# Optimization experiments

Measured on AMD Instinct MI355X. Metric: run time of the kernel, lower is better.

Reference implementation:

```python
import jax, jax.numpy as jnp
import numpy as np

BATCH, IN, OUT = 8192, 4096, 4096


def setup_inputs() -> dict:
    key = jax.random.key(0)
    k1, k2, k3 = jax.random.split(key, 3)
    x = jax.random.normal(k1, (BATCH, IN), dtype=jnp.float32)
    weight = jax.random.normal(k2, (OUT, IN), dtype=jnp.float32)
    bias = jax.random.normal(k3, (OUT,), dtype=jnp.float32)
    return {"x": x, "weight": weight, "bias": bias}


def reference(x, weight, bias):
    # Binarize weights/bias with sign (matches torch.sign: sign(0)=0), then fp32 GEMM + bias add.
    w = jnp.sign(weight)            # [OUT, IN], values in {-1, 0, +1}
    b = jnp.sign(bias)              # [OUT]
    return jnp.dot(x, w.T) + b[None, :]   # [BATCH, OUT]
```

## Files before the change

### kernel.cpp

```cpp
#include <hip/hip_runtime.h>
#include <stdint.h>
#include <stddef.h>


#define MDIM 8192
#define NDIM 4096
#define KDIM 4096
#define NT   (KDIM / 64)

typedef __attribute__((ext_vector_type(8))) short bf16x8;
typedef __attribute__((ext_vector_type(4))) float f32x4;

__device__ __forceinline__ short f2bf(float f) {
  union { float f; unsigned u; } a; a.f = f;
  unsigned r = a.u + 0x7FFFu + ((a.u >> 16) & 1u);
  return (short)(r >> 16);
}

__device__ __forceinline__ float fsign(float x) {
  return (x > 0.f) ? 1.f : ((x < 0.f) ? -1.f : 0.f);
}

__device__ __forceinline__ short signbf(float x) {
  return (x > 0.f) ? (short)0x3F80 : ((x < 0.f) ? (short)0xBF80 : (short)0);
}

__device__ __forceinline__ void gl_lds16(const void* g, void* l) {
  __builtin_amdgcn_global_load_lds(
      (const __attribute__((address_space(1))) unsigned*)g,
      (__attribute__((address_space(3))) unsigned*)l,
      16, 0, 0);
}


__global__ void cvt_x_kernel(const float* __restrict__ x, short* __restrict__ o) {
  int i = blockIdx.x * blockDim.x + threadIdx.x;
  float4 v = ((const float4*)x)[i];
  short4 s;
  s.x = f2bf(v.x); s.y = f2bf(v.y); s.z = f2bf(v.z); s.w = f2bf(v.w);
  ((short4*)o)[i] = s;
}

__global__ void cvt_w_kernel(const float* __restrict__ w, short* __restrict__ o) {
  int i = blockIdx.x * blockDim.x + threadIdx.x;
  float4 v = ((const float4*)w)[i];
  short4 s;
  s.x = signbf(v.x); s.y = signbf(v.y); s.z = signbf(v.z); s.w = signbf(v.w);
  ((short4*)o)[i] = s;
}


#define STAGE(BUF, HH, KTS) do {                                               \
    const short* _s = ((HH) < 2 ? aA + (size_t)((HH) * 128) * KDIM             \
                                : aB + (size_t)(((HH) - 2) * 128) * KDIM)      \
                      + (size_t)(KTS) * 64;                                    \
    char* _d = ldst + (BUF) * 65536 + (HH) * 16384;                            \
    gl_lds16(_s, _d);                                                          \
    gl_lds16(_s + (size_t)64 * KDIM, _d + 8192);                               \
  } while (0)

#define READ_A(QOFF) do {                                                      \
    _Pragma("unroll") for (int i = 0; i < 4; ++i) {                            \
      const int ro = so + arow + (QOFF) + i * 2048;                            \
      a[i][0] = *(const bf16x8*)(sm + ro + colp0);                             \
      a[i][1] = *(const bf16x8*)(sm + ro + colp1);                             \
    } } while (0)

#define READ_B(DST, QOFF) do {                                                 \
    _Pragma("unroll") for (int j = 0; j < 2; ++j) {                            \
      const int ro = so + brow + (QOFF) + j * 2048;                            \
      DST[j][0] = *(const bf16x8*)(sm + ro + colp0);                           \
      DST[j][1] = *(const bf16x8*)(sm + ro + colp1);                           \
    } } while (0)

#define MFMA_Q(I0, J0, BREG) do {                                              \
    __builtin_amdgcn_s_setprio(1);                                            \
    _Pragma("unroll") for (int i = 0; i < 4; ++i)                              \
      _Pragma("unroll") for (int j = 0; j < 2; ++j) {                          \
        acc[(I0) + i][(J0) + j] = __builtin_amdgcn_mfma_f32_16x16x32_bf16(     \
            a[i][0], BREG[j][0], acc[(I0) + i][(J0) + j], 0, 0, 0);            \
        acc[(I0) + i][(J0) + j] = __builtin_amdgcn_mfma_f32_16x16x32_bf16(     \
            a[i][1], BREG[j][1], acc[(I0) + i][(J0) + j], 0, 0, 0);            \
      }                                                                        \
    __builtin_amdgcn_s_setprio(0);                                            \
  } while (0)

#define SYNC_PRE_MFMA() do {                                                   \
    __builtin_amdgcn_s_barrier();                                              \
    asm volatile("s_waitcnt lgkmcnt(0)" ::: "memory");                         \
    __builtin_amdgcn_sched_barrier(0);                                         \
  } while (0)

__global__ __launch_bounds__(512, 2) void gemm_8phase(
    const short* __restrict__ A,
    const short* __restrict__ B,
    const float* __restrict__ bias,
    float* __restrict__ C) {
  __shared__ __align__(16) char sm[131072];

  const int t    = threadIdx.x;
  const int lane = t & 63;
  const int w    = t >> 6;
  const int wm   = w >> 2;
  const int wn   = w & 3;
  const int fr   = lane & 15;
  const int g    = lane >> 4;

  const int bid = blockIdx.y * gridDim.x + blockIdx.x;
  const int swz = (bid & 7) * 64 + (bid >> 3);
  const int bm  = (swz >> 4) << 8;
  const int bn  = (swz & 15) << 8;

  const int sx    = (fr & 7) << 4;
  const int colp0 = (g << 4) ^ sx;
  const int colp1 = (64 | (g << 4)) ^ sx;
  const int arow  = (wm * 128 + fr) * 128;
  const int brow  = 32768 + (wn * 64 + fr) * 128;

  const int srow = t >> 3;
  const int scol = ((t & 7) ^ (srow & 7)) << 3;
  const short* aA = A + (size_t)(bm + srow) * KDIM + scol;
  const short* aB = B + (size_t)(bn + srow) * KDIM + scol;
  char* ldst = (char*)sm + t * 16;

  f32x4 acc[8][4] = {};
  bf16x8 a[4][2], b0[2][2], b1[2][2];

  STAGE(0, 0, 0);
  STAGE(0, 1, 0);
  STAGE(0, 2, 0);
  STAGE(0, 3, 0);
  STAGE(1, 0, 1);
  asm volatile("s_waitcnt vmcnt(2)" ::: "memory");
  __builtin_amdgcn_s_barrier();

  for (int kt = 0; kt < NT; ++kt) {
    const int so = (kt & 1) << 16;
    const int nb = (kt & 1) ^ 1;
    const int cb = (kt & 1);

    READ_A(0);
    READ_B(b0, 0);
    if (kt + 1 < NT) STAGE(nb, 1, kt + 1);
    SYNC_PRE_MFMA();
    MFMA_Q(0, 0, b0);
    __builtin_amdgcn_s_barrier();

    READ_B(b1, 4096);
    if (kt + 1 < NT) STAGE(nb, 2, kt + 1);
    SYNC_PRE_MFMA();
    MFMA_Q(0, 2, b1);
    __builtin_amdgcn_s_barrier();

    READ_A(8192);
    if (kt + 1 < NT) STAGE(nb, 3, kt + 1);
    SYNC_PRE_MFMA();
    MFMA_Q(4, 2, b1);
    __builtin_amdgcn_s_barrier();

    if (kt + 2 < NT) STAGE(cb, 0, kt + 2);
    __builtin_amdgcn_s_barrier();
    MFMA_Q(4, 0, b0);
    if (kt + 2 < NT) {
      asm volatile("s_waitcnt vmcnt(2)" ::: "memory");
    } else {
      asm volatile("s_waitcnt vmcnt(0)" ::: "memory");
    }
    __builtin_amdgcn_s_barrier();
  }

  const int crow = bm + wm * 128;
  const int ccol = bn + wn * 64 + fr;
#pragma unroll
  for (int jj = 0; jj < 4; ++jj) {
    const int gc = ccol + jj * 16;
    const float bs = fsign(bias[gc]);
#pragma unroll
    for (int ii = 0; ii < 8; ++ii) {
      float* cp = C + (size_t)(crow + ii * 16 + g * 4) * NDIM + gc;
#pragma unroll
      for (int r = 0; r < 4; ++r)
        cp[(size_t)r * NDIM] = acc[ii][jj][r] + bs;
    }
  }
}


__global__ __launch_bounds__(256) void gemm_fused(
    const float* __restrict__ A,
    const float* __restrict__ W,
    const float* __restrict__ bias,
    float* __restrict__ C) {
  __shared__ short As[128 * 32];
  __shared__ short Bs[128 * 32];

  const int t    = threadIdx.x;
  const int lane = t & 63;
  const int wm   = (t >> 6) >> 1;
  const int wn   = (t >> 6) & 1;

  const int bm = blockIdx.y * 128;
  const int bn = blockIdx.x * 128;

  f32x4 acc[4][4] = {};

  const int srow = t >> 1;
  const int scol = (t & 1) << 4;

  const float* pA = A + (size_t)(bm + srow) * KDIM + scol;
  const float* pW = W + (size_t)(bn + srow) * KDIM + scol;
  short* sA = As + srow * 32 + scol;
  short* sB = Bs + srow * 32 + scol;

  const int fr  = lane & 15;
  const int fkB = (lane >> 4) << 4;

  for (int k0 = 0; k0 < KDIM; k0 += 32) {
    float4 va[4], vb[4];
#pragma unroll
    for (int q = 0; q < 4; ++q) {
      va[q] = *(const float4*)(pA + k0 + q * 4);
      vb[q] = *(const float4*)(pW + k0 + q * 4);
    }
    __syncthreads();
    short va_s[16], vb_s[16];
#pragma unroll
    for (int q = 0; q < 4; ++q) {
      va_s[q * 4 + 0] = f2bf(va[q].x); va_s[q * 4 + 1] = f2bf(va[q].y);
      va_s[q * 4 + 2] = f2bf(va[q].z); va_s[q * 4 + 3] = f2bf(va[q].w);
      vb_s[q * 4 + 0] = signbf(vb[q].x); vb_s[q * 4 + 1] = signbf(vb[q].y);
      vb_s[q * 4 + 2] = signbf(vb[q].z); vb_s[q * 4 + 3] = signbf(vb[q].w);
    }
    bf16x8 ca, cbv;
#pragma unroll
    for (int e = 0; e < 8; ++e) { ca[e] = va_s[e]; cbv[e] = vb_s[e]; }
    *(bf16x8*)(sA) = ca;
    *(bf16x8*)(sB) = cbv;
#pragma unroll
    for (int e = 0; e < 8; ++e) { ca[e] = va_s[8 + e]; cbv[e] = vb_s[8 + e]; }
    *(bf16x8*)(sA + 8) = ca;
    *(bf16x8*)(sB + 8) = cbv;
    __syncthreads();

    bf16x8 af[4], bfr[4];
#pragma unroll
    for (int i = 0; i < 4; ++i) {
      af[i]  = *(const bf16x8*)((const char*)As + (wm * 64 + i * 16 + fr) * 64 + fkB);
      bfr[i] = *(const bf16x8*)((const char*)Bs + (wn * 64 + i * 16 + fr) * 64 + fkB);
    }
#pragma unroll
    for (int i = 0; i < 4; ++i)
#pragma unroll
      for (int j = 0; j < 4; ++j)
        acc[i][j] = __builtin_amdgcn_mfma_f32_16x16x32_bf16(af[i], bfr[j], acc[i][j], 0, 0, 0);
  }
  __syncthreads();

  const int row0 = bm + wm * 64 + ((lane >> 4) << 2);
  const int col0 = bn + wn * 64 + (lane & 15);
#pragma unroll
  for (int j = 0; j < 4; ++j) {
    const int gc = col0 + j * 16;
    const float bs = fsign(bias[gc]);
#pragma unroll
    for (int i = 0; i < 4; ++i) {
      float* cp = C + (size_t)(row0 + i * 16) * NDIM + gc;
#pragma unroll
      for (int r = 0; r < 4; ++r)
        cp[(size_t)r * NDIM] = acc[i][j][r] + bs;
    }
  }
}

extern "C" void kernel_launch(void* const* d_in, const int* in_sizes, int n_in,
                              void* d_out, int out_size, void* d_ws, size_t ws_size,
                              hipStream_t stream) {
  const float* x    = (const float*)d_in[0];
  const float* w    = (const float*)d_in[1];
  const float* bias = (const float*)d_in[2];
  float* out = (float*)d_out;

  const size_t xb_bytes = (size_t)MDIM * KDIM * 2;
  const size_t wb_bytes = (size_t)NDIM * KDIM * 2;

  if (ws_size >= xb_bytes + wb_bytes) {
    short* xb = (short*)d_ws;
    short* wb = (short*)((char*)d_ws + xb_bytes);
    cvt_x_kernel<<<(MDIM * (KDIM / 4)) / 256, 256, 0, stream>>>(x, xb);
    cvt_w_kernel<<<(NDIM * (KDIM / 4)) / 256, 256, 0, stream>>>(w, wb);
    dim3 grid(NDIM / 256, MDIM / 256);
    gemm_8phase<<<grid, 512, 0, stream>>>(xb, wb, bias, out);
  } else {
    dim3 grid(NDIM / 128, MDIM / 128);
    gemm_fused<<<grid, 256, 0, stream>>>(x, w, bias, out);
  }
}
```

Measured before the change: 478.6 us.

## Restructure GEMM main loop into unrolled two-tile software pipeline with register prefetch

The K loop is rewritten as a macro-unrolled pair of tiles. It uses separate A register sets (a1/a2) so that LDS reads for the next tile's A-low and B0 fragments are issued during the current tile's MFMA phases. Global-to-LDS staging now runs two tiles ahead for all four quarters, and the explicit lgkmcnt waits and sched_barriers are dropped in favour of plain barriers. The aim is to hide LDS read latency and remove the per-phase drain stalls. The cost is more vector registers, and correctness depends on the compiler inserting the right lgkmcnt waits and on the new vmcnt accounting.

```diff
diff --git a/kernel.cpp b/kernel.cpp
--- a/kernel.cpp
+++ b/kernel.cpp
@@ -49,6 +49,11 @@
   ((short4*)o)[i] = s;
 }
 
+
+#define BAR() __builtin_amdgcn_s_barrier()
+#define VM2 asm volatile("s_waitcnt vmcnt(2)" ::: "memory")
+#define VM0 asm volatile("s_waitcnt vmcnt(0)" ::: "memory")
+#define VMNONE
 
 #define STAGE(BUF, HH, KTS) do {                                               \
     const short* _s = ((HH) < 2 ? aA + (size_t)((HH) * 128) * KDIM             \
@@ -59,36 +64,71 @@
     gl_lds16(_s + (size_t)64 * KDIM, _d + 8192);                               \
   } while (0)
 
-#define READ_A(QOFF) do {                                                      \
+#define READ_ALO(SO) do {                                                      \
     _Pragma("unroll") for (int i = 0; i < 4; ++i) {                            \
-      const int ro = so + arow + (QOFF) + i * 2048;                            \
-      a[i][0] = *(const bf16x8*)(sm + ro + colp0);                             \
-      a[i][1] = *(const bf16x8*)(sm + ro + colp1);                             \
+      const int ro = (SO) + arow + i * 2048;                                   \
+      a1[i][0] = *(const bf16x8*)(sm + ro + colp0);                            \
+      a1[i][1] = *(const bf16x8*)(sm + ro + colp1);                            \
     } } while (0)
 
-#define READ_B(DST, QOFF) do {                                                 \
+#define READ_AHI(SO) do {                                                      \
+    _Pragma("unroll") for (int i = 0; i < 4; ++i) {                            \
+      const int ro = (SO) + arow + 8192 + i * 2048;                            \
+      a2[i][0] = *(const bf16x8*)(sm + ro + colp0);                            \
+      a2[i][1] = *(const bf16x8*)(sm + ro + colp1);                            \
+    } } while (0)
+
+#define READ_B0v(SO) do {                                                      \
     _Pragma("unroll") for (int j = 0; j < 2; ++j) {                            \
-      const int ro = so + brow + (QOFF) + j * 2048;                            \
-      DST[j][0] = *(const bf16x8*)(sm + ro + colp0);                           \
-      DST[j][1] = *(const bf16x8*)(sm + ro + colp1);                           \
+      const int ro = (SO) + brow + j * 2048;                                   \
+      b0[j][0] = *(const bf16x8*)(sm + ro + colp0);                            \
+      b0[j][1] = *(const bf16x8*)(sm + ro + colp1);                            \
     } } while (0)
 
-#define MFMA_Q(I0, J0, BREG) do {                                              \
+#define READ_B1v(SO) do {                                                      \
+    _Pragma("unroll") for (int j = 0; j < 2; ++j) {                            \
+      const int ro = (SO) + brow + 4096 + j * 2048;                            \
+      b1[j][0] = *(const bf16x8*)(sm + ro + colp0);                            \
+      b1[j][1] = *(const bf16x8*)(sm + ro + colp1);                            \
+    } } while (0)
+
+#define MFMA_Q(I0, J0, AV, BV) do {                                            \
     __builtin_amdgcn_s_setprio(1);                                            \
     _Pragma("unroll") for (int i = 0; i < 4; ++i)                              \
       _Pragma("unroll") for (int j = 0; j < 2; ++j) {                          \
         acc[(I0) + i][(J0) + j] = __builtin_amdgcn_mfma_f32_16x16x32_bf16(     \
-            a[i][0], BREG[j][0], acc[(I0) + i][(J0) + j], 0, 0, 0);            \
+            AV[i][0], BV[j][0], acc[(I0) + i][(J0) + j], 0, 0, 0);             \
         acc[(I0) + i][(J0) + j] = __builtin_amdgcn_mfma_f32_16x16x32_bf16(     \
-            a[i][1], BREG[j][1], acc[(I0) + i][(J0) + j], 0, 0, 0);            \
+            AV[i][1], BV[j][1], acc[(I0) + i][(J0) + j], 0, 0, 0);             \
       }                                                                        \
     __builtin_amdgcn_s_setprio(0);                                            \
   } while (0)
 
-#define SYNC_PRE_MFMA() do {                                                   \
-    __builtin_amdgcn_s_barrier();                                              \
-    asm volatile("s_waitcnt lgkmcnt(0)" ::: "memory");                         \
-    __builtin_amdgcn_sched_barrier(0);                                         \
+#define KTILE(SOC, SON, BC, KT, DS, DP, VMOP) do {                             \
+                                                                      \
+    READ_B1v(SOC);                                                             \
+    BAR();                                                                     \
+    MFMA_Q(0, 0, a1, b0);                                                      \
+    BAR();                                                                     \
+                                                                      \
+    READ_AHI(SOC);                                                             \
+    if (DS) STAGE(BC, 2, (KT) + 2);                                            \
+    BAR();                                                                     \
+    MFMA_Q(0, 2, a1, b1);                                                      \
+    VMOP;                                                                      \
+    BAR();                                                                     \
+                                                                      \
+    if (DP) READ_ALO(SON);                                                     \
+    if (DS) { STAGE(BC, 3, (KT) + 2); STAGE(BC, 1, (KT) + 2); }                \
+    BAR();                                                                     \
+    MFMA_Q(4, 2, a2, b1);                                                      \
+    BAR();                                                                     \
+                                                                      \
+    if (DS) STAGE(BC, 0, (KT) + 2);                                            \
+    BAR();                                                                     \
+    MFMA_Q(4, 0, a2, b0);                                                      \
+    if (DP) READ_B0v(SON);                                                     \
+    BAR();                                                                     \
   } while (0)
 
 __global__ __launch_bounds__(512, 2) void gemm_8phase(
@@ -124,50 +164,21 @@
   char* ldst = (char*)sm + t * 16;
 
   f32x4 acc[8][4] = {};
-  bf16x8 a[4][2], b0[2][2], b1[2][2];
-
-  STAGE(0, 0, 0);
-  STAGE(0, 1, 0);
-  STAGE(0, 2, 0);
-  STAGE(0, 3, 0);
-  STAGE(1, 0, 1);
-  asm volatile("s_waitcnt vmcnt(2)" ::: "memory");
-  __builtin_amdgcn_s_barrier();
-
-  for (int kt = 0; kt < NT; ++kt) {
-    const int so = (kt & 1) << 16;
-    const int nb = (kt & 1) ^ 1;
-    const int cb = (kt & 1);
-
-    READ_A(0);
-    READ_B(b0, 0);
-    if (kt + 1 < NT) STAGE(nb, 1, kt + 1);
-    SYNC_PRE_MFMA();
-    MFMA_Q(0, 0, b0);
-    __builtin_amdgcn_s_barrier();
-
-    READ_B(b1, 4096);
-    if (kt + 1 < NT) STAGE(nb, 2, kt + 1);
-    SYNC_PRE_MFMA();
-    MFMA_Q(0, 2, b1);
-    __builtin_amdgcn_s_barrier();
-
-    READ_A(8192);
-    if (kt + 1 < NT) STAGE(nb, 3, kt + 1);
-    SYNC_PRE_MFMA();
-    MFMA_Q(4, 2, b1);
-    __builtin_amdgcn_s_barrier();
-
-    if (kt + 2 < NT) STAGE(cb, 0, kt + 2);
-    __builtin_amdgcn_s_barrier();
-    MFMA_Q(4, 0, b0);
-    if (kt + 2 < NT) {
-      asm volatile("s_waitcnt vmcnt(2)" ::: "memory");
-    } else {
-      asm volatile("s_waitcnt vmcnt(0)" ::: "memory");
-    }
-    __builtin_amdgcn_s_barrier();
-  }
+  bf16x8 a1[4][2], a2[4][2], b0[2][2], b1[2][2];
+
+  STAGE(0, 0, 0); STAGE(0, 1, 0); STAGE(0, 2, 0); STAGE(0, 3, 0);
+  STAGE(1, 2, 1); STAGE(1, 3, 1); STAGE(1, 1, 1); STAGE(1, 0, 1);
+  asm volatile("s_waitcnt vmcnt(8)" ::: "memory");
+  BAR();
+  READ_ALO(0);
+  READ_B0v(0);
+
+  for (int kt = 0; kt < NT - 2; kt += 2) {
+    KTILE(0,     65536, 0, kt,     1, 1, VM2);
+    KTILE(65536, 0,     1, kt + 1, 1, 1, VM2);
+  }
+  KTILE(0,     65536, 0, NT - 2, 0, 1, VM0);
+  KTILE(65536, 0,     1, NT - 1, 0, 0, VMNONE);
 
   const int crow = bm + wm * 128;
   const int ccol = bn + wn * 64 + fr;
```

Measured after the change: 932.1 us. 1.95x slower.
